# Kernel optimization log

Measured on AMD Instinct MI355X. Metric: run time of the kernel, lower is better.

Reference implementation:

```python
import jax, jax.numpy as jnp
import numpy as np

B, G = 2, 64  # batch, voxel grid edge

def setup_inputs() -> dict:
    key = jax.random.key(0)
    k1, k2 = jax.random.split(key)
    alphatensor = jax.random.normal(k1, (B, 3, 3, G, G, G), dtype=jnp.float32)
    C0_4 = jax.random.normal(k2, (3, 3, 3, 3), dtype=jnp.float32)
    return {"alphatensor": alphatensor, "C0_4": C0_4}

def reference(alphatensor, C0_4):
    # Original math: C_ijkl[b,x,y,z] = sum_{mnop} a_mi a_nj a_ok a_pl C0_mnop
    # (torch code builds a rank-8 Gtensor outer product then contracts; we do
    #  the same contraction as four staged rank-4 contractions — identical result.)
    a = alphatensor
    t = jnp.einsum('bmixyz,mnop->bnopixyz', a, C0_4)   # contract m
    t = jnp.einsum('bnjxyz,bnopixyz->bopijxyz', a, t)  # contract n
    t = jnp.einsum('bokxyz,bopijxyz->bpijkxyz', a, t)  # contract o
    C = jnp.einsum('bplxyz,bpijkxyz->bijklxyz', a, t)  # contract p
    return C
```

## Files before the change

kernel.cpp:

```cpp
#include <hip/hip_runtime.h>


#define GRIDE 64
#define NVOX (GRIDE * GRIDE * GRIDE)
#define NV4  (NVOX / 4)
#define NB 2

typedef float nfloat4 __attribute__((ext_vector_type(4)));

__device__ __forceinline__ float4 f4mulV(float4 a, float4 b) {
    float4 r; r.x = a.x * b.x; r.y = a.y * b.y; r.z = a.z * b.z; r.w = a.w * b.w; return r;
}
__device__ __forceinline__ float4 f4fmaV(float4 a, float4 b, float4 acc) {
    acc.x = fmaf(a.x, b.x, acc.x); acc.y = fmaf(a.y, b.y, acc.y);
    acc.z = fmaf(a.z, b.z, acc.z); acc.w = fmaf(a.w, b.w, acc.w); return acc;
}
__device__ __forceinline__ float4 f4fmaS(float4 v, float s, float4 acc) {
    acc.x = fmaf(v.x, s, acc.x); acc.y = fmaf(v.y, s, acc.y);
    acc.z = fmaf(v.z, s, acc.z); acc.w = fmaf(v.w, s, acc.w); return acc;
}
__device__ __forceinline__ float4 f4mulS(float4 v, float s) {
    float4 r; r.x = v.x * s; r.y = v.y * s; r.z = v.z * s; r.w = v.w * s; return r;
}
__device__ __forceinline__ void ntStore(float4* p, float4 v) {
    nfloat4 nv; nv.x = v.x; nv.y = v.y; nv.z = v.z; nv.w = v.w;
    __builtin_nontemporal_store(nv, (nfloat4*)p);
}

__global__ __launch_bounds__(256, 3) void alphaC0_kernel(
    const float4* __restrict__ a,
    const float*  __restrict__ c0,
    float4* __restrict__ out)
{
    const int t = blockIdx.x * blockDim.x + threadIdx.x;
    const int b = t >> 16;
    const int vg = t & (NV4 - 1);

    const float4* __restrict__ ab = a + (size_t)b * 9 * NV4 + vg;
    float4 A[3][3];
#pragma unroll
    for (int m = 0; m < 3; ++m)
#pragma unroll
        for (int i = 0; i < 3; ++i)
            A[m][i] = ab[(m * 3 + i) * NV4];

    float4* __restrict__ ob = out + (size_t)b * 81 * NV4 + vg;

#pragma unroll
    for (int i = 0; i < 3; ++i) {
#pragma unroll
        for (int j = 0; j < 3; ++j) {
            float4 M[3][3];
#pragma unroll
            for (int m = 0; m < 3; ++m)
#pragma unroll
                for (int n = 0; n < 3; ++n)
                    M[m][n] = f4mulV(A[m][i], A[n][j]);

            float4 t2[3][3];
#pragma unroll
            for (int o = 0; o < 3; ++o)
#pragma unroll
                for (int p = 0; p < 3; ++p) {
                    float4 s = f4mulS(M[0][0], c0[((0 * 3 + 0) * 3 + o) * 3 + p]);
#pragma unroll
                    for (int m = 0; m < 3; ++m)
#pragma unroll
                        for (int n = 0; n < 3; ++n)
                            if (m || n)
                                s = f4fmaS(M[m][n], c0[((m * 3 + n) * 3 + o) * 3 + p], s);
                    t2[o][p] = s;
                }

#pragma unroll
            for (int k = 0; k < 3; ++k) {
                float4 t3[3];
#pragma unroll
                for (int p = 0; p < 3; ++p) {
                    float4 s = f4mulV(A[0][k], t2[0][p]);
                    s = f4fmaV(A[1][k], t2[1][p], s);
                    s = f4fmaV(A[2][k], t2[2][p], s);
                    t3[p] = s;
                }

#pragma unroll
                for (int l = 0; l < 3; ++l) {
                    float4 s = f4mulV(A[0][l], t3[0]);
                    s = f4fmaV(A[1][l], t3[1], s);
                    s = f4fmaV(A[2][l], t3[2], s);
                    ntStore(&ob[(((i * 3 + j) * 3 + k) * 3 + l) * NV4], s);
                }
            }
        }
    }
}

extern "C" void kernel_launch(void* const* d_in, const int* in_sizes, int n_in,
                              void* d_out, int out_size, void* d_ws, size_t ws_size,
                              hipStream_t stream) {
    const float4* a  = (const float4*)d_in[0];
    const float*  c0 = (const float*)d_in[1];
    float4* out = (float4*)d_out;

    const int total = NB * NV4;
    const int block = 256;
    const int grid = total / block;
    alphaC0_kernel<<<grid, block, 0, stream>>>(a, c0, out);
}
```

Baseline: 188.6 us.

## Split output (i,j) pairs across blocks to raise parallelism

Each block now computes only one (i,j) slice of the 81 outputs for a chunk of voxels, so the grid grows ninefold and each thread does a ninth of the work and stores. This is meant to expose more concurrent waves and memory-level parallelism for the store-heavy kernel. In exchange, every input voxel is reloaded nine times, and the c0 contraction is recomputed per block.

```diff
diff --git a/kernel.cpp b/kernel.cpp
--- a/kernel.cpp
+++ b/kernel.cpp
@@ -5,6 +5,7 @@
 #define NVOX (GRIDE * GRIDE * GRIDE)
 #define NV4  (NVOX / 4)
 #define NB 2
+#define CHUNKS 256
 
 typedef float nfloat4 __attribute__((ext_vector_type(4)));
 
@@ -32,65 +33,70 @@
     const float*  __restrict__ c0,
     float4* __restrict__ out)
 {
-    const int t = blockIdx.x * blockDim.x + threadIdx.x;
-    const int b = t >> 16;
-    const int vg = t & (NV4 - 1);
+    const int bid = blockIdx.x;
+    const int g = bid >> 8;
+    const int chunk = bid & (CHUNKS - 1);
+    const int vg = chunk * 256 + threadIdx.x;
+    const int b = g / 9;
+    const int ij = g % 9;
+    const int i = ij / 3, j = ij % 3;
 
     const float4* __restrict__ ab = a + (size_t)b * 9 * NV4 + vg;
+
     float4 A[3][3];
 #pragma unroll
     for (int m = 0; m < 3; ++m)
 #pragma unroll
-        for (int i = 0; i < 3; ++i)
-            A[m][i] = ab[(m * 3 + i) * NV4];
+        for (int c = 0; c < 3; ++c)
+            A[m][c] = ab[(m * 3 + c) * NV4];
 
-    float4* __restrict__ ob = out + (size_t)b * 81 * NV4 + vg;
+    float4 Ai[3], Aj[3];
+#pragma unroll
+    for (int m = 0; m < 3; ++m) {
+        Ai[m] = (i == 0) ? A[m][0] : ((i == 1) ? A[m][1] : A[m][2]);
+        Aj[m] = (j == 0) ? A[m][0] : ((j == 1) ? A[m][1] : A[m][2]);
+    }
 
+    float4 M[3][3];
 #pragma unroll
-    for (int i = 0; i < 3; ++i) {
+    for (int m = 0; m < 3; ++m)
 #pragma unroll
-        for (int j = 0; j < 3; ++j) {
-            float4 M[3][3];
+        for (int n = 0; n < 3; ++n)
+            M[m][n] = f4mulV(Ai[m], Aj[n]);
+
+    float4 t2[3][3];
+#pragma unroll
+    for (int o = 0; o < 3; ++o)
+#pragma unroll
+        for (int p = 0; p < 3; ++p) {
+            float4 s = f4mulS(M[0][0], c0[((0 * 3 + 0) * 3 + o) * 3 + p]);
 #pragma unroll
             for (int m = 0; m < 3; ++m)
 #pragma unroll
                 for (int n = 0; n < 3; ++n)
-                    M[m][n] = f4mulV(A[m][i], A[n][j]);
+                    if (m || n)
+                        s = f4fmaS(M[m][n], c0[((m * 3 + n) * 3 + o) * 3 + p], s);
+            t2[o][p] = s;
+        }
 
-            float4 t2[3][3];
-#pragma unroll
-            for (int o = 0; o < 3; ++o)
-#pragma unroll
-                for (int p = 0; p < 3; ++p) {
-                    float4 s = f4mulS(M[0][0], c0[((0 * 3 + 0) * 3 + o) * 3 + p]);
-#pragma unroll
-                    for (int m = 0; m < 3; ++m)
-#pragma unroll
-                        for (int n = 0; n < 3; ++n)
-                            if (m || n)
-                                s = f4fmaS(M[m][n], c0[((m * 3 + n) * 3 + o) * 3 + p], s);
-                    t2[o][p] = s;
-                }
+    float4* __restrict__ ob = out + ((size_t)b * 81 + ij * 9) * NV4 + vg;
 
 #pragma unroll
-            for (int k = 0; k < 3; ++k) {
-                float4 t3[3];
+    for (int k = 0; k < 3; ++k) {
+        float4 t3[3];
 #pragma unroll
-                for (int p = 0; p < 3; ++p) {
-                    float4 s = f4mulV(A[0][k], t2[0][p]);
-                    s = f4fmaV(A[1][k], t2[1][p], s);
-                    s = f4fmaV(A[2][k], t2[2][p], s);
-                    t3[p] = s;
-                }
-
+        for (int p = 0; p < 3; ++p) {
+            float4 s = f4mulV(A[0][k], t2[0][p]);
+            s = f4fmaV(A[1][k], t2[1][p], s);
+            s = f4fmaV(A[2][k], t2[2][p], s);
+            t3[p] = s;
+        }
 #pragma unroll
-                for (int l = 0; l < 3; ++l) {
-                    float4 s = f4mulV(A[0][l], t3[0]);
-                    s = f4fmaV(A[1][l], t3[1], s);
-                    s = f4fmaV(A[2][l], t3[2], s);
-                    ntStore(&ob[(((i * 3 + j) * 3 + k) * 3 + l) * NV4], s);
-                }
-            }
+        for (int l = 0; l < 3; ++l) {
+            float4 s = f4mulV(A[0][l], t3[0]);
+            s = f4fmaV(A[1][l], t3[1], s);
+            s = f4fmaV(A[2][l], t3[2], s);
+            ntStore(&ob[(k * 3 + l) * NV4], s);
         }
     }
 }
@@ -102,8 +108,6 @@
     const float*  c0 = (const float*)d_in[1];
     float4* out = (float4*)d_out;
 
-    const int total = NB * NV4;
-    const int block = 256;
-    const int grid = total / block;
-    alphaC0_kernel<<<grid, block, 0, stream>>>(a, c0, out);
+    const int grid = NB * 9 * CHUNKS;
+    alphaC0_kernel<<<grid, 256, 0, stream>>>(a, c0, out);
 }
```

Result: slower. 254.0 us (+34.6%).
